# Performance work log

Measured on AMD Instinct MI355X. Metric: run time of the kernel, lower is better.

Reference implementation:

```python
import jax, jax.numpy as jnp
import numpy as np
import jax.ops

N = 100000   # nodes
E = 3200000  # edges
B = 256      # graphs in batch
F_IN, H, C = 128, 64, 2


def gcn_conv(x, src, dst, W, b):
    # PyG GCNConv: x' = D^{-1/2} (A + I) D^{-1/2} (x W) + b
    n = x.shape[0]
    h = x @ W  # [N, H]
    loop = jnp.arange(n)
    s = jnp.concatenate([src, loop])  # add self-loops
    d = jnp.concatenate([dst, loop])
    deg = jax.ops.segment_sum(jnp.ones_like(d, dtype=h.dtype), d, num_segments=n)
    dinv = jnp.where(deg > 0, jax.lax.rsqrt(deg), 0.0)
    norm = dinv[s] * dinv[d]  # [E+N]
    msg = h[s] * norm[:, None]  # gather + scale
    out = jax.ops.segment_sum(msg, d, num_segments=n)  # scatter-add
    return out + b


def setup_inputs() -> dict:
    key = jax.random.key(0)
    ks = jax.random.split(key, 10)
    x = jax.random.normal(ks[0], (N, F_IN), dtype=jnp.float32)
    edge_index = jax.random.randint(ks[1], (2, E), 0, N, dtype=jnp.int64)
    batch = jnp.sort(jax.random.randint(ks[2], (N,), 0, B, dtype=jnp.int64))
    glorot = lambda k, fi, fo: jax.random.uniform(k, (fi, fo), jnp.float32, -1, 1) * np.sqrt(6.0 / (fi + fo))
    return {
        "x": x, "edge_index": edge_index, "batch": batch,
        "W1": glorot(ks[3], F_IN, H), "b1": jnp.zeros((H,), jnp.float32),
        "W2": glorot(ks[4], H, H), "b2": jnp.zeros((H,), jnp.float32),
        "Wl": glorot(ks[5], H, C), "bl": jnp.zeros((C,), jnp.float32),
    }


def reference(x, edge_index, batch, W1, b1, W2, b2, Wl, bl):
    src, dst = edge_index[0], edge_index[1]
    h = jax.nn.relu(gcn_conv(x, src, dst, W1, b1))
    h = jax.nn.relu(gcn_conv(h, src, dst, W2, b2))
    # global_mean_pool over graph ids
    sums = jax.ops.segment_sum(h, batch, num_segments=B)
    cnt = jax.ops.segment_sum(jnp.ones((h.shape[0],), h.dtype), batch, num_segments=B)
    pooled = sums / jnp.maximum(cnt, 1.0)[:, None]  # [B, H]
    return pooled @ Wl + bl  # [B, C]
```

## Files before the change

### kernel.cpp

```cpp
#include <hip/hip_runtime.h>
#include <hip/hip_bf16.h>


#define HDIM 64
#define NB 256
#define SGRID 256

typedef __attribute__((ext_vector_type(8))) short short8;
typedef __attribute__((ext_vector_type(4))) float f32x4;
union FragU { uint4 u; short8 s; };

static __device__ __forceinline__ unsigned bf16_bits(float f) {
    unsigned u = __float_as_uint(f);
    return (u + 0x7fff + ((u >> 16) & 1)) >> 16;
}
static __device__ __forceinline__ float bflo(unsigned w) { return __uint_as_float(w << 16); }
static __device__ __forceinline__ float bfhi(unsigned w) { return __uint_as_float(w & 0xffff0000u); }


__global__ __launch_bounds__(1024) void k_bcount(const int* __restrict__ dst,
        int* __restrict__ blkhist, int E, int npb, int chunk) {
    __shared__ int lh[NB];
    int tid = threadIdx.x;
    if (tid < NB) lh[tid] = 0;
    __syncthreads();
    int e0 = blockIdx.x * chunk, e1 = min(E, e0 + chunk);
    for (int e = e0 + tid; e < e1; e += 1024)
        atomicAdd(&lh[(unsigned)dst[e] / (unsigned)npb], 1);
    __syncthreads();
    if (tid < NB) blkhist[blockIdx.x * NB + tid] = lh[tid];
}

__global__ void k_bscan2(int* __restrict__ blkhist, int* __restrict__ bcnt) {
    __shared__ int s[SGRID];
    int b = blockIdx.x, t = threadIdx.x;
    int orig = blkhist[t * NB + b];
    s[t] = orig;
    __syncthreads();
    for (int off = 1; off < SGRID; off <<= 1) {
        int v = 0;
        if (t >= off) v = s[t - off];
        __syncthreads();
        s[t] += v;
        __syncthreads();
    }
    blkhist[t * NB + b] = s[t] - orig;
    if (t == SGRID - 1) bcnt[b] = s[t];
}

__global__ void k_bscan(const int* __restrict__ bcnt, int* __restrict__ bstart) {
    if (threadIdx.x == 0) {
        int s = 0;
        for (int i = 0; i < NB; ++i) { bstart[i] = s; s += bcnt[i]; }
        bstart[NB] = s;
    }
}

__global__ __launch_bounds__(1024) void k_bscatter(const int* __restrict__ src,
        const int* __restrict__ dst, const int* __restrict__ bstart,
        const int* __restrict__ blkhist, unsigned* __restrict__ ebuf,
        int E, int npb, int chunk) {
    __shared__ int base[NB], lcur[NB];
    int tid = threadIdx.x;
    if (tid < NB) {
        base[tid] = bstart[tid] + blkhist[blockIdx.x * NB + tid];
        lcur[tid] = 0;
    }
    __syncthreads();
    int e0 = blockIdx.x * chunk, e1 = min(E, e0 + chunk);
    for (int e = e0 + tid; e < e1; e += 1024) {
        int d = dst[e];
        unsigned b = (unsigned)d / (unsigned)npb;
        unsigned ld = (unsigned)d - b * (unsigned)npb;
        int off = atomicAdd(&lcur[b], 1);
        ebuf[base[b] + off] = (ld << 17) | (unsigned)src[e];
    }
}

__global__ __launch_bounds__(1024) void k_bfill(const unsigned* __restrict__ ebuf,
        const int* __restrict__ bucket_start, int* __restrict__ row_start,
        int* __restrict__ cnt, float* __restrict__ dinv, int* __restrict__ csr,
        int N, int npb) {
    __shared__ int h[512], p[512], c[512];
    int b = blockIdx.x, tid = threadIdx.x;
    int vlo = b * npb;
    int vcnt = min(npb, N - vlo);
    if (vcnt <= 0) return;
    for (int i = tid; i < 512; i += 1024) h[i] = 0;
    __syncthreads();
    int e0 = bucket_start[b], e1 = bucket_start[b + 1];
    for (int e = e0 + tid; e < e1; e += 1024)
        atomicAdd(&h[ebuf[e] >> 17], 1);
    __syncthreads();
    if (tid < 512) p[tid] = h[tid];
    __syncthreads();
    for (int off = 1; off < 512; off <<= 1) {
        int v = 0;
        if (tid < 512 && tid >= off) v = p[tid - off];
        __syncthreads();
        if (tid < 512) p[tid] += v;
        __syncthreads();
    }
    if (tid < vcnt) {
        int excl = p[tid] - h[tid];
        int v = vlo + tid;
        row_start[v] = e0 + excl;
        cnt[v] = h[tid];
        dinv[v] = rsqrtf((float)(h[tid] + 1));
        c[tid] = excl;
    }
    __syncthreads();
    for (int e = e0 + tid; e < e1; e += 1024) {
        unsigned ed = ebuf[e];
        int off = atomicAdd(&c[ed >> 17], 1);
        csr[e0 + off] = (int)(ed & 0x1FFFFu);
    }
}

__global__ void k_prep(const float* __restrict__ W1, const float* __restrict__ W2,
                       uint4* __restrict__ W1s, uint4* __restrict__ W2s) {
    int t = threadIdx.x;
    int lane = t & 63, ci = t >> 6;
    {
        int kt = ci >> 2, nt = ci & 3;
        int kbase = kt * 32 + (lane >> 4) * 8;
        int n = nt * 16 + (lane & 15);
        uint4 o;
        unsigned* op = (unsigned*)&o;
        for (int jj = 0; jj < 4; ++jj) {
            unsigned lo = bf16_bits(W1[(kbase + 2 * jj) * 64 + n]);
            unsigned hi = bf16_bits(W1[(kbase + 2 * jj + 1) * 64 + n]);
            op[jj] = lo | (hi << 16);
        }
        W1s[ci * 64 + lane] = o;
    }
    if (ci < 8) {
        int kt = ci >> 2, nt = ci & 3;
        int kbase = kt * 32 + (lane >> 4) * 8;
        int n = nt * 16 + (lane & 15);
        uint4 o;
        unsigned* op = (unsigned*)&o;
        for (int jj = 0; jj < 4; ++jj) {
            unsigned lo = bf16_bits(W2[(kbase + 2 * jj) * 64 + n]);
            unsigned hi = bf16_bits(W2[(kbase + 2 * jj + 1) * 64 + n]);
            op[jj] = lo | (hi << 16);
        }
        W2s[ci * 64 + lane] = o;
    }
}

#define MFMA_EPILOGUE(OUT)                                                     \
    {                                                                          \
        int col = lane & 15;                                                   \
        float dv[4];                                                           \
        for (int r = 0; r < 4; ++r) {                                          \
            int vr = v0 + quad * 4 + r;                                        \
            dv[r] = dinv[vr < n ? vr : (n - 1)];                               \
        }                                                                      \
        for (int nt = 0; nt < 4; ++nt)                                         \
            for (int r = 0; r < 4; ++r) {                                      \
                int vr = v0 + quad * 4 + r;                                    \
                float val = acc[nt][r] * dv[r];                                \
                float oth = __shfl_xor(val, 1, 64);                            \
                if (!(lane & 1) && vr < n)                                     \
                    OUT[(size_t)vr * 32 + nt * 8 + (col >> 1)] =               \
                        bf16_bits(val) | (bf16_bits(oth) << 16);               \
            }                                                                  \
    }

__global__ __launch_bounds__(256) void k_mgemm1(const float* __restrict__ X,
        const uint4* __restrict__ W1s, const float* __restrict__ dinv,
        unsigned* __restrict__ hsb, int n) {
    int lane = threadIdx.x & 63, wv = threadIdx.x >> 6;
    int v0 = (blockIdx.x * 4 + wv) * 16;
    if (v0 >= n) return;
    int quad = lane >> 4;
    int vm = v0 + (lane & 15); if (vm >= n) vm = n - 1;
    const float* xr = X + (size_t)vm * 128 + quad * 8;
    f32x4 acc[4] = {f32x4{0,0,0,0}, f32x4{0,0,0,0}, f32x4{0,0,0,0}, f32x4{0,0,0,0}};
#pragma unroll
    for (int kt = 0; kt < 4; ++kt) {
        float4 xa = *(const float4*)(xr + kt * 32);
        float4 xb = *(const float4*)(xr + kt * 32 + 4);
        FragU a;
        a.u.x = bf16_bits(xa.x) | (bf16_bits(xa.y) << 16);
        a.u.y = bf16_bits(xa.z) | (bf16_bits(xa.w) << 16);
        a.u.z = bf16_bits(xb.x) | (bf16_bits(xb.y) << 16);
        a.u.w = bf16_bits(xb.z) | (bf16_bits(xb.w) << 16);
#pragma unroll
        for (int nt = 0; nt < 4; ++nt) {
            FragU b; b.u = W1s[(kt * 4 + nt) * 64 + lane];
            acc[nt] = __builtin_amdgcn_mfma_f32_16x16x32_bf16(a.s, b.s, acc[nt], 0, 0, 0);
        }
    }
    MFMA_EPILOGUE(hsb)
}

__global__ __launch_bounds__(256) void k_mgemm2(const unsigned* __restrict__ h1b,
        const uint4* __restrict__ W2s, const float* __restrict__ dinv,
        unsigned* __restrict__ hsbB, int n) {
    int lane = threadIdx.x & 63, wv = threadIdx.x >> 6;
    int v0 = (blockIdx.x * 4 + wv) * 16;
    if (v0 >= n) return;
    int quad = lane >> 4;
    int vm = v0 + (lane & 15); if (vm >= n) vm = n - 1;
    const uint4* h4 = (const uint4*)h1b;
    f32x4 acc[4] = {f32x4{0,0,0,0}, f32x4{0,0,0,0}, f32x4{0,0,0,0}, f32x4{0,0,0,0}};
#pragma unroll
    for (int kt = 0; kt < 2; ++kt) {
        FragU a; a.u = h4[(size_t)vm * 8 + kt * 4 + quad];
#pragma unroll
        for (int nt = 0; nt < 4; ++nt) {
            FragU b; b.u = W2s[(kt * 4 + nt) * 64 + lane];
            acc[nt] = __builtin_amdgcn_mfma_f32_16x16x32_bf16(a.s, b.s, acc[nt], 0, 0, 0);
        }
    }
    MFMA_EPILOGUE(hsbB)
}

#define GATHER_BODY                                                            \
    const uint4* hs4p = (const uint4*)hsb;                                     \
    int o = lane & 7, oct = lane >> 3;                                         \
    float a0=0.f,a1=0.f,a2=0.f,a3=0.f,a4=0.f,a5=0.f,a6=0.f,a7=0.f;             \
    if (oct == 0) {                                                            \
        uint4 s = hs4p[(size_t)v * 8 + o];                                     \
        a0=bflo(s.x);a1=bfhi(s.x);a2=bflo(s.y);a3=bfhi(s.y);                   \
        a4=bflo(s.z);a5=bfhi(s.z);a6=bflo(s.w);a7=bfhi(s.w);                   \
    }                                                                          \
    int rs = row_start[v], c = cnt[v];                                         \
    int base = 0;                                                              \
    for (; base + 64 <= c; base += 64) {                                       \
        int idx = csr[rs + base + lane];                                       \
        uint4 wbuf[8];                                                         \
        _Pragma("unroll")                                                      \
        for (int jj = 0; jj < 8; ++jj) {                                       \
            int u = __shfl(idx, jj * 8 + oct, 64);                             \
            wbuf[jj] = hs4p[(size_t)u * 8 + o];                                \
        }                                                                      \
        _Pragma("unroll")                                                      \
        for (int jj = 0; jj < 8; ++jj) {                                       \
            a0+=bflo(wbuf[jj].x);a1+=bfhi(wbuf[jj].x);                         \
            a2+=bflo(wbuf[jj].y);a3+=bfhi(wbuf[jj].y);                         \
            a4+=bflo(wbuf[jj].z);a5+=bfhi(wbuf[jj].z);                         \
            a6+=bflo(wbuf[jj].w);a7+=bfhi(wbuf[jj].w);                         \
        }                                                                      \
    }                                                                          \
    if (base < c) {                                                            \
        int m = c - base;                                                      \
        int idx = (lane < m) ? csr[rs + base + lane] : 0;                      \
        for (int j = 0; j < m; j += 8) {                                       \
            int u = __shfl(idx, j + oct, 64);                                  \
            if (j + oct < m) {                                                 \
                uint4 wn = hs4p[(size_t)u * 8 + o];                            \
                a0+=bflo(wn.x);a1+=bfhi(wn.x);a2+=bflo(wn.y);a3+=bfhi(wn.y);   \
                a4+=bflo(wn.z);a5+=bfhi(wn.z);a6+=bflo(wn.w);a7+=bfhi(wn.w);   \
            }                                                                  \
        }                                                                      \
    }                                                                          \
    a0+=__shfl_xor(a0,8,64);a0+=__shfl_xor(a0,16,64);a0+=__shfl_xor(a0,32,64); \
    a1+=__shfl_xor(a1,8,64);a1+=__shfl_xor(a1,16,64);a1+=__shfl_xor(a1,32,64); \
    a2+=__shfl_xor(a2,8,64);a2+=__shfl_xor(a2,16,64);a2+=__shfl_xor(a2,32,64); \
    a3+=__shfl_xor(a3,8,64);a3+=__shfl_xor(a3,16,64);a3+=__shfl_xor(a3,32,64); \
    a4+=__shfl_xor(a4,8,64);a4+=__shfl_xor(a4,16,64);a4+=__shfl_xor(a4,32,64); \
    a5+=__shfl_xor(a5,8,64);a5+=__shfl_xor(a5,16,64);a5+=__shfl_xor(a5,32,64); \
    a6+=__shfl_xor(a6,8,64);a6+=__shfl_xor(a6,16,64);a6+=__shfl_xor(a6,32,64); \
    a7+=__shfl_xor(a7,8,64);a7+=__shfl_xor(a7,16,64);a7+=__shfl_xor(a7,32,64); \
    float dv = dinv[v];                                                        \
    float4 bb0 = ((const float4*)bias)[2 * o];                                 \
    float4 bb1 = ((const float4*)bias)[2 * o + 1];                             \
    float r0 = fmaxf(fmaf(dv, a0, bb0.x), 0.f);                                \
    float r1 = fmaxf(fmaf(dv, a1, bb0.y), 0.f);                                \
    float r2 = fmaxf(fmaf(dv, a2, bb0.z), 0.f);                                \
    float r3 = fmaxf(fmaf(dv, a3, bb0.w), 0.f);                                \
    float r4 = fmaxf(fmaf(dv, a4, bb1.x), 0.f);                                \
    float r5 = fmaxf(fmaf(dv, a5, bb1.y), 0.f);                                \
    float r6 = fmaxf(fmaf(dv, a6, bb1.z), 0.f);                                \
    float r7 = fmaxf(fmaf(dv, a7, bb1.w), 0.f);

__global__ void k_conv1(const unsigned* __restrict__ hsb, const int* __restrict__ row_start,
                        const int* __restrict__ cnt, const int* __restrict__ csr,
                        const float* __restrict__ dinv, const float* __restrict__ bias,
                        unsigned* __restrict__ h1b, int n) {
    int v = (blockIdx.x * 256 + threadIdx.x) >> 6;
    int lane = threadIdx.x & 63;
    if (v >= n) return;
    GATHER_BODY
    if (oct == 0) {
        uint4 pk;
        pk.x = bf16_bits(r0) | (bf16_bits(r1) << 16);
        pk.y = bf16_bits(r2) | (bf16_bits(r3) << 16);
        pk.z = bf16_bits(r4) | (bf16_bits(r5) << 16);
        pk.w = bf16_bits(r6) | (bf16_bits(r7) << 16);
        ((uint4*)h1b)[(size_t)v * 8 + o] = pk;
    }
}

__global__ void k_conv_out(const unsigned* __restrict__ hsb, const int* __restrict__ row_start,
                           const int* __restrict__ cnt, const int* __restrict__ csr,
                           const float* __restrict__ dinv, const float* __restrict__ bias,
                           const float* __restrict__ Wl, float2* __restrict__ z, int n) {
    int v = (blockIdx.x * 256 + threadIdx.x) >> 6;
    int lane = threadIdx.x & 63;
    if (v >= n) return;
    GATHER_BODY
    const float4* Wl4 = (const float4*)Wl;
    float4 wA = Wl4[4 * o + 0];
    float4 wB = Wl4[4 * o + 1];
    float4 wC = Wl4[4 * o + 2];
    float4 wD = Wl4[4 * o + 3];
    float c0 = r0*wA.x + r1*wA.z + r2*wB.x + r3*wB.z + r4*wC.x + r5*wC.z + r6*wD.x + r7*wD.z;
    float c1 = r0*wA.y + r1*wA.w + r2*wB.y + r3*wB.w + r4*wC.y + r5*wC.w + r6*wD.y + r7*wD.w;
    c0 += __shfl_xor(c0, 1, 64); c1 += __shfl_xor(c1, 1, 64);
    c0 += __shfl_xor(c0, 2, 64); c1 += __shfl_xor(c1, 2, 64);
    c0 += __shfl_xor(c0, 4, 64); c1 += __shfl_xor(c1, 4, 64);
    if (lane == 0) z[v] = make_float2(c0, c1);
}

static __device__ __forceinline__ int lower_bound(const int* __restrict__ a, int n, int key) {
    int lo = 0, hi = n;
    while (lo < hi) {
        int mid = (lo + hi) >> 1;
        if (a[mid] < key) lo = mid + 1; else hi = mid;
    }
    return lo;
}

__global__ void k_pool_z(const float2* __restrict__ z, const int* __restrict__ batch,
                         const float* __restrict__ bl, float* __restrict__ out, int N, int B) {
    int g = (blockIdx.x * 256 + threadIdx.x) >> 6;
    int lane = threadIdx.x & 63;
    if (g >= B) return;
    int lo = lower_bound(batch, N, g);
    int hi = lower_bound(batch, N, g + 1);
    float c0 = 0.f, c1 = 0.f;
    for (int v = lo + lane; v < hi; v += 64) {
        float2 t = z[v];
        c0 += t.x; c1 += t.y;
    }
    #pragma unroll
    for (int off = 32; off; off >>= 1) {
        c0 += __shfl_xor(c0, off, 64);
        c1 += __shfl_xor(c1, off, 64);
    }
    if (lane == 0) {
        float inv = 1.0f / fmaxf((float)(hi - lo), 1.0f);
        out[g * 2 + 0] = c0 * inv + bl[0];
        out[g * 2 + 1] = c1 * inv + bl[1];
    }
}

extern "C" void kernel_launch(void* const* d_in, const int* in_sizes, int n_in,
                              void* d_out, int out_size, void* d_ws, size_t ws_size,
                              hipStream_t stream) {
    const float* x  = (const float*)d_in[0];
    const int* edge = (const int*)d_in[1];
    const int* batch= (const int*)d_in[2];
    const float* W1 = (const float*)d_in[3];
    const float* b1 = (const float*)d_in[4];
    const float* W2 = (const float*)d_in[5];
    const float* b2 = (const float*)d_in[6];
    const float* Wl = (const float*)d_in[7];
    const float* bl = (const float*)d_in[8];
    float* out = (float*)d_out;

    const int N = in_sizes[2];
    const int E = in_sizes[1] / 2;
    const int B = out_size / 2;
    const int* srcp = edge;
    const int* dstp = edge + E;
    const int npb = (N + NB - 1) / NB;

    char* w = (char*)d_ws;
    auto carve = [&](size_t bytes) { void* p = (void*)w; w += (bytes + 255) & ~(size_t)255; return p; };
    int*      cnt     = (int*)carve((size_t)N * 4);
    int*      rsA     = (int*)carve((size_t)N * 4);
    float*    dinv    = (float*)carve((size_t)N * 4);
    int*      bcnt    = (int*)carve((NB + 8) * 4);
    int*      bstart  = (int*)carve((NB + 8) * 4);
    int*      blkhist = (int*)carve((size_t)SGRID * NB * 4);
    uint4*    W1s     = (uint4*)carve(16 * 64 * 16);
    uint4*    W2s     = (uint4*)carve(8 * 64 * 16);
    int*      csr     = (int*)carve((size_t)E * 4);
    unsigned* ebuf    = (unsigned*)carve((size_t)E * 4);
    unsigned* hsbA    = (unsigned*)carve((size_t)N * 32 * 4);
    unsigned* h1b     = (unsigned*)carve((size_t)N * 32 * 4);
    unsigned* hsbB    = (unsigned*)carve((size_t)N * 32 * 4);
    float2*   zbuf    = (float2*)carve((size_t)N * 8);

    const int chunk = (E + SGRID - 1) / SGRID;
    int wbl = (N + 3) / 4;
    int gbl = (N + 63) / 64;

    k_prep<<<1, 1024, 0, stream>>>(W1, W2, W1s, W2s);
    k_bcount<<<SGRID, 1024, 0, stream>>>(dstp, blkhist, E, npb, chunk);
    k_bscan2<<<NB, SGRID, 0, stream>>>(blkhist, bcnt);
    k_bscan<<<1, 64, 0, stream>>>(bcnt, bstart);
    k_bscatter<<<SGRID, 1024, 0, stream>>>(srcp, dstp, bstart, blkhist, ebuf, E, npb, chunk);
    k_bfill<<<NB, 1024, 0, stream>>>(ebuf, bstart, rsA, cnt, dinv, csr, N, npb);

    k_mgemm1<<<gbl, 256, 0, stream>>>(x, W1s, dinv, hsbA, N);
    k_conv1<<<wbl, 256, 0, stream>>>(hsbA, rsA, cnt, csr, dinv, b1, h1b, N);
    k_mgemm2<<<gbl, 256, 0, stream>>>(h1b, W2s, dinv, hsbB, N);
    k_conv_out<<<wbl, 256, 0, stream>>>(hsbB, rsA, cnt, csr, dinv, b2, Wl, zbuf, N);

    k_pool_z<<<(B * 64 + 255) / 256, 256, 0, stream>>>(zbuf, batch, bl, out, N, B);
}
```

Before: 378.4 us.

## Pad CSR rows to multiples of eight with zero-row sentinel to simplify gather

Each node's CSR row is padded up to a multiple of 8 entries, and the padding points at an extra all-zero sentinel row N in the feature buffers. This lets the gather loop work in uniform groups of 8 neighbours with no separate tail path. The serial bucket-start scan becomes a parallel shared-memory scan, and ebuf now aliases hsbA to save workspace. The cost is extra padded gathers of the zero row, extra fill writes in k_bfill, and a larger CSR array.

```diff
diff --git a/kernel.cpp b/kernel.cpp
--- a/kernel.cpp
+++ b/kernel.cpp
@@ -49,11 +49,20 @@
 }
 
 __global__ void k_bscan(const int* __restrict__ bcnt, int* __restrict__ bstart) {
-    if (threadIdx.x == 0) {
-        int s = 0;
-        for (int i = 0; i < NB; ++i) { bstart[i] = s; s += bcnt[i]; }
-        bstart[NB] = s;
-    }
+    __shared__ int s[NB];
+    int t = threadIdx.x;
+    int orig = bcnt[t];
+    s[t] = orig;
+    __syncthreads();
+    for (int off = 1; off < NB; off <<= 1) {
+        int v = 0;
+        if (t >= off) v = s[t - off];
+        __syncthreads();
+        s[t] += v;
+        __syncthreads();
+    }
+    bstart[t] = s[t] - orig;
+    if (t == NB - 1) bstart[NB] = s[t];
 }
 
 __global__ __launch_bounds__(1024) void k_bscatter(const int* __restrict__ src,
@@ -78,8 +87,8 @@
 }
 
 __global__ __launch_bounds__(1024) void k_bfill(const unsigned* __restrict__ ebuf,
-        const int* __restrict__ bucket_start, int* __restrict__ row_start,
-        int* __restrict__ cnt, float* __restrict__ dinv, int* __restrict__ csr,
+        const int* __restrict__ bstart, int* __restrict__ row_start,
+        int* __restrict__ cnt8, float* __restrict__ dinv, int* __restrict__ csr,
         int N, int npb) {
     __shared__ int h[512], p[512], c[512];
     int b = blockIdx.x, tid = threadIdx.x;
@@ -88,11 +97,15 @@
     if (vcnt <= 0) return;
     for (int i = tid; i < 512; i += 1024) h[i] = 0;
     __syncthreads();
-    int e0 = bucket_start[b], e1 = bucket_start[b + 1];
+    int e0 = bstart[b], e1 = bstart[b + 1];
     for (int e = e0 + tid; e < e1; e += 1024)
         atomicAdd(&h[ebuf[e] >> 17], 1);
     __syncthreads();
-    if (tid < 512) p[tid] = h[tid];
+    int pc = 0;
+    if (tid < 512) {
+        pc = (tid < vcnt) ? ((h[tid] + 7) & ~7) : 0;
+        p[tid] = pc;
+    }
     __syncthreads();
     for (int off = 1; off < 512; off <<= 1) {
         int v = 0;
@@ -101,11 +114,12 @@
         if (tid < 512) p[tid] += v;
         __syncthreads();
     }
+    int bb = e0 + 7 * vlo;
     if (tid < vcnt) {
-        int excl = p[tid] - h[tid];
+        int excl = p[tid] - pc;
         int v = vlo + tid;
-        row_start[v] = e0 + excl;
-        cnt[v] = h[tid];
+        row_start[v] = bb + excl;
+        cnt8[v] = pc >> 3;
         dinv[v] = rsqrtf((float)(h[tid] + 1));
         c[tid] = excl;
     }
@@ -113,12 +127,18 @@
     for (int e = e0 + tid; e < e1; e += 1024) {
         unsigned ed = ebuf[e];
         int off = atomicAdd(&c[ed >> 17], 1);
-        csr[e0 + off] = (int)(ed & 0x1FFFFu);
+        csr[bb + off] = (int)(ed & 0x1FFFFu);
+    }
+    __syncthreads();
+    if (tid < vcnt) {
+        int excl = p[tid] - pc;
+        for (int q = excl + h[tid]; q < excl + pc; ++q) csr[bb + q] = N;
     }
 }
 
 __global__ void k_prep(const float* __restrict__ W1, const float* __restrict__ W2,
-                       uint4* __restrict__ W1s, uint4* __restrict__ W2s) {
+                       uint4* __restrict__ W1s, uint4* __restrict__ W2s,
+                       unsigned* __restrict__ hsbA, unsigned* __restrict__ hsbB, int N) {
     int t = threadIdx.x;
     int lane = t & 63, ci = t >> 6;
     {
@@ -147,6 +167,8 @@
         }
         W2s[ci * 64 + lane] = o;
     }
+    if (t < 32) hsbA[(size_t)N * 32 + t] = 0;
+    else if (t < 64) hsbB[(size_t)N * 32 + (t - 32)] = 0;
 }
 
 #define MFMA_EPILOGUE(OUT)                                                     \
@@ -227,35 +249,25 @@
         a0=bflo(s.x);a1=bfhi(s.x);a2=bflo(s.y);a3=bfhi(s.y);                   \
         a4=bflo(s.z);a5=bfhi(s.z);a6=bflo(s.w);a7=bfhi(s.w);                   \
     }                                                                          \
-    int rs = row_start[v], c = cnt[v];                                         \
-    int base = 0;                                                              \
-    for (; base + 64 <= c; base += 64) {                                       \
-        int idx = csr[rs + base + lane];                                       \
-        uint4 wbuf[8];                                                         \
+    int rs = row_start[v], nb = cnt8[v];                                       \
+    for (int base = 0; base < nb; base += 8) {                                 \
+        int idx = csr[rs + base * 8 + lane];   \
+        int m = nb - base; if (m > 8) m = 8;                 \
+        uint4 wb[8];                                                           \
         _Pragma("unroll")                                                      \
-        for (int jj = 0; jj < 8; ++jj) {                                       \
-            int u = __shfl(idx, jj * 8 + oct, 64);                             \
-            wbuf[jj] = hs4p[(size_t)u * 8 + o];                                \
-        }                                                                      \
+        for (int i = 0; i < 8; ++i)                                            \
+            if (i < m) {                                                       \
+                int u = __shfl(idx, i * 8 + oct, 64);                          \
+                wb[i] = hs4p[(size_t)u * 8 + o];                               \
+            }                                                                  \
         _Pragma("unroll")                                                      \
-        for (int jj = 0; jj < 8; ++jj) {                                       \
-            a0+=bflo(wbuf[jj].x);a1+=bfhi(wbuf[jj].x);                         \
-            a2+=bflo(wbuf[jj].y);a3+=bfhi(wbuf[jj].y);                         \
-            a4+=bflo(wbuf[jj].z);a5+=bfhi(wbuf[jj].z);                         \
-            a6+=bflo(wbuf[jj].w);a7+=bfhi(wbuf[jj].w);                         \
-        }                                                                      \
-    }                                                                          \
-    if (base < c) {                                                            \
-        int m = c - base;                                                      \
-        int idx = (lane < m) ? csr[rs + base + lane] : 0;                      \
-        for (int j = 0; j < m; j += 8) {                                       \
-            int u = __shfl(idx, j + oct, 64);                                  \
-            if (j + oct < m) {                                                 \
-                uint4 wn = hs4p[(size_t)u * 8 + o];                            \
-                a0+=bflo(wn.x);a1+=bfhi(wn.x);a2+=bflo(wn.y);a3+=bfhi(wn.y);   \
-                a4+=bflo(wn.z);a5+=bfhi(wn.z);a6+=bflo(wn.w);a7+=bfhi(wn.w);   \
+        for (int i = 0; i < 8; ++i)                                            \
+            if (i < m) {                                                       \
+                a0+=bflo(wb[i].x);a1+=bfhi(wb[i].x);                           \
+                a2+=bflo(wb[i].y);a3+=bfhi(wb[i].y);                           \
+                a4+=bflo(wb[i].z);a5+=bfhi(wb[i].z);                           \
+                a6+=bflo(wb[i].w);a7+=bfhi(wb[i].w);                           \
             }                                                                  \
-        }                                                                      \
     }                                                                          \
     a0+=__shfl_xor(a0,8,64);a0+=__shfl_xor(a0,16,64);a0+=__shfl_xor(a0,32,64); \
     a1+=__shfl_xor(a1,8,64);a1+=__shfl_xor(a1,16,64);a1+=__shfl_xor(a1,32,64); \
@@ -278,7 +290,7 @@
     float r7 = fmaxf(fmaf(dv, a7, bb1.w), 0.f);
 
 __global__ void k_conv1(const unsigned* __restrict__ hsb, const int* __restrict__ row_start,
-                        const int* __restrict__ cnt, const int* __restrict__ csr,
+                        const int* __restrict__ cnt8, const int* __restrict__ csr,
                         const float* __restrict__ dinv, const float* __restrict__ bias,
                         unsigned* __restrict__ h1b, int n) {
     int v = (blockIdx.x * 256 + threadIdx.x) >> 6;
@@ -296,7 +308,7 @@
 }
 
 __global__ void k_conv_out(const unsigned* __restrict__ hsb, const int* __restrict__ row_start,
-                           const int* __restrict__ cnt, const int* __restrict__ csr,
+                           const int* __restrict__ cnt8, const int* __restrict__ csr,
                            const float* __restrict__ dinv, const float* __restrict__ bias,
                            const float* __restrict__ Wl, float2* __restrict__ z, int n) {
     int v = (blockIdx.x * 256 + threadIdx.x) >> 6;
@@ -372,7 +384,7 @@
 
     char* w = (char*)d_ws;
     auto carve = [&](size_t bytes) { void* p = (void*)w; w += (bytes + 255) & ~(size_t)255; return p; };
-    int*      cnt     = (int*)carve((size_t)N * 4);
+    int*      cnt8    = (int*)carve((size_t)N * 4);
     int*      rsA     = (int*)carve((size_t)N * 4);
     float*    dinv    = (float*)carve((size_t)N * 4);
     int*      bcnt    = (int*)carve((NB + 8) * 4);
@@ -380,28 +392,28 @@
     int*      blkhist = (int*)carve((size_t)SGRID * NB * 4);
     uint4*    W1s     = (uint4*)carve(16 * 64 * 16);
     uint4*    W2s     = (uint4*)carve(8 * 64 * 16);
-    int*      csr     = (int*)carve((size_t)E * 4);
-    unsigned* ebuf    = (unsigned*)carve((size_t)E * 4);
-    unsigned* hsbA    = (unsigned*)carve((size_t)N * 32 * 4);
-    unsigned* h1b     = (unsigned*)carve((size_t)N * 32 * 4);
-    unsigned* hsbB    = (unsigned*)carve((size_t)N * 32 * 4);
+    int*      csr     = (int*)carve(((size_t)E + 7 * (size_t)N + 256) * 4);
+    unsigned* hsbA    = (unsigned*)carve(((size_t)N + 1) * 32 * 4);
+    unsigned* ebuf    = hsbA;
+    unsigned* h1b     = (unsigned*)carve(((size_t)N + 1) * 32 * 4);
+    unsigned* hsbB    = (unsigned*)carve(((size_t)N + 1) * 32 * 4);
     float2*   zbuf    = (float2*)carve((size_t)N * 8);
 
     const int chunk = (E + SGRID - 1) / SGRID;
     int wbl = (N + 3) / 4;
     int gbl = (N + 63) / 64;
 
-    k_prep<<<1, 1024, 0, stream>>>(W1, W2, W1s, W2s);
     k_bcount<<<SGRID, 1024, 0, stream>>>(dstp, blkhist, E, npb, chunk);
     k_bscan2<<<NB, SGRID, 0, stream>>>(blkhist, bcnt);
-    k_bscan<<<1, 64, 0, stream>>>(bcnt, bstart);
+    k_bscan<<<1, NB, 0, stream>>>(bcnt, bstart);
     k_bscatter<<<SGRID, 1024, 0, stream>>>(srcp, dstp, bstart, blkhist, ebuf, E, npb, chunk);
-    k_bfill<<<NB, 1024, 0, stream>>>(ebuf, bstart, rsA, cnt, dinv, csr, N, npb);
+    k_bfill<<<NB, 1024, 0, stream>>>(ebuf, bstart, rsA, cnt8, dinv, csr, N, npb);
+    k_prep<<<1, 1024, 0, stream>>>(W1, W2, W1s, W2s, hsbA, hsbB, N);
 
     k_mgemm1<<<gbl, 256, 0, stream>>>(x, W1s, dinv, hsbA, N);
-    k_conv1<<<wbl, 256, 0, stream>>>(hsbA, rsA, cnt, csr, dinv, b1, h1b, N);
+    k_conv1<<<wbl, 256, 0, stream>>>(hsbA, rsA, cnt8, csr, dinv, b1, h1b, N);
     k_mgemm2<<<gbl, 256, 0, stream>>>(h1b, W2s, dinv, hsbB, N);
-    k_conv_out<<<wbl, 256, 0, stream>>>(hsbB, rsA, cnt, csr, dinv, b2, Wl, zbuf, N);
+    k_conv_out<<<wbl, 256, 0, stream>>>(hsbB, rsA, cnt8, csr, dinv, b2, Wl, zbuf, N);
 
     k_pool_z<<<(B * 64 + 255) / 256, 256, 0, stream>>>(zbuf, batch, bl, out, N, B);
 }
```

New measurement: 324.9 us. 1.16x faster.
